# Kernel optimization log

Measured on AMD Instinct MI355X. Metric: run time of the kernel, lower is better.

Reference implementation:

```python
import math
import jax, jax.numpy as jnp
import numpy as np

CAPACITY_FACTOR = 1.0
MIN_CAPACITY = 8


def setup_inputs() -> dict:
    key = jax.random.key(0)
    k1, k2 = jax.random.split(key)
    s, d, e = 8192, 1024, 64
    inputs = jax.random.normal(k1, (s, d), dtype=jnp.float32)
    wg_weight = jax.random.normal(k2, (e, d), dtype=jnp.float32) * (1.0 / math.sqrt(d))
    return {"inputs": inputs, "wg_weight": wg_weight}


def reference(inputs, wg_weight):
    # gate projection (always fp32 in the original)
    logits = inputs.astype(jnp.float32) @ wg_weight.T  # [s, e]
    s, e = logits.shape
    # static capacity: ceil(s/e * capacity_factor), floored at min_capacity
    capacity = max(int(math.ceil(s / e * CAPACITY_FACTOR)), MIN_CAPACITY)

    gates = jax.nn.softmax(logits, axis=1)            # [s, e]
    indices = jnp.argmax(gates, axis=1)               # [s]
    mask = jax.nn.one_hot(indices, e, dtype=jnp.int32)  # [s, e]
    exp_counts = jnp.sum(mask, axis=0)                # [e]

    # load-balancing aux loss (uses mask BEFORE capacity dropping)
    me = jnp.mean(gates, axis=0)
    ce = jnp.mean(mask.astype(jnp.float32), axis=0)
    l_aux = jnp.sum(me * ce) * e

    # capacity dropping: with use_rts=False, topk over the binary mask keeps
    # the first `capacity` tokens routed to each expert, i.e. cumulative
    # position-in-expert < capacity
    positions = jnp.cumsum(mask, axis=0) - 1          # [s, e]
    mask = mask * (positions < capacity).astype(jnp.int32)

    locations = jnp.cumsum(mask, axis=0) - 1          # [s, e]
    locations_s = jnp.sum(locations * mask, axis=1)   # [s] slot per token

    gates = gates * mask.astype(jnp.float32)          # zero out dropped tokens
    locations_sc = jax.nn.one_hot(locations_s, capacity, dtype=jnp.float32)  # [s, c]
    combine_weights = jnp.einsum('se,sc->sec', gates, locations_sc)  # [s, e, c]
    dispatch_mask = combine_weights.astype(bool)
    return l_aux, combine_weights, dispatch_mask, exp_counts
```

## Files before the change

### kernel.cpp

```cpp
#include <hip/hip_runtime.h>
#include <cstdint>
#include <cstddef>

#define S 8192
#define Dm 1024
#define E 64
#define CAP 128
#define SEC 67108864ull

#define GEMM_BLOCKS 256
#define FILL_BLOCKS 1792

typedef float f32x4 __attribute__((ext_vector_type(4)));

__global__ __launch_bounds__(256) void k_main(const float* __restrict__ x,
                                              const float* __restrict__ w,
                                              float* __restrict__ gate,
                                              int* __restrict__ idx,
                                              float* __restrict__ me_part,
                                              float* __restrict__ out) {
    int bid = blockIdx.x;
    int tid = threadIdx.x;
    if (bid < GEMM_BLOCKS) {
        __shared__ float Al[32][66];
        __shared__ float Wl[64][68];
        __shared__ float sm[32];
        __shared__ float sinv[32];
        int tok = tid & 31;
        int eo = tid >> 5;
        int t0 = bid * 32;
        const float* asrc = x + (size_t)(t0 + (tid >> 3)) * Dm + (tid & 7) * 8;
        const float* wsrc0 = w + (size_t)(tid >> 3) * Dm + (tid & 7) * 8;
        const float* wsrc1 = wsrc0 + 32 * (size_t)Dm;
        float* adst = &Al[tid >> 3][(tid & 7) * 8];
        float* wdst0 = &Wl[tid >> 3][(tid & 7) * 8];
        float* wdst1 = &Wl[32 + (tid >> 3)][(tid & 7) * 8];

        float acc[8] = {0.f, 0.f, 0.f, 0.f, 0.f, 0.f, 0.f, 0.f};
        float4 pa0 = *(const float4*)(asrc + 0);
        float4 pa1 = *(const float4*)(asrc + 4);
        float4 pw0 = *(const float4*)(wsrc0 + 0);
        float4 pw1 = *(const float4*)(wsrc0 + 4);
        float4 pw2 = *(const float4*)(wsrc1 + 0);
        float4 pw3 = *(const float4*)(wsrc1 + 4);

        for (int ch = 0; ch < 16; ++ch) {
            __syncthreads();
            *(float2*)(adst + 0) = make_float2(pa0.x, pa0.y);
            *(float2*)(adst + 2) = make_float2(pa0.z, pa0.w);
            *(float2*)(adst + 4) = make_float2(pa1.x, pa1.y);
            *(float2*)(adst + 6) = make_float2(pa1.z, pa1.w);
            *(float4*)(wdst0 + 0) = pw0;
            *(float4*)(wdst0 + 4) = pw1;
            *(float4*)(wdst1 + 0) = pw2;
            *(float4*)(wdst1 + 4) = pw3;
            __syncthreads();
            if (ch < 15) {
                int kb = (ch + 1) * 64;
                pa0 = *(const float4*)(asrc + kb);
                pa1 = *(const float4*)(asrc + kb + 4);
                pw0 = *(const float4*)(wsrc0 + kb);
                pw1 = *(const float4*)(wsrc0 + kb + 4);
                pw2 = *(const float4*)(wsrc1 + kb);
                pw3 = *(const float4*)(wsrc1 + kb + 4);
            }
#pragma unroll 4
            for (int k4 = 0; k4 < 16; ++k4) {
                float2 aa = *(const float2*)&Al[tok][k4 * 4];
                float2 ab = *(const float2*)&Al[tok][k4 * 4 + 2];
#pragma unroll
                for (int j = 0; j < 8; ++j) {
                    float4 wv = *(const float4*)&Wl[eo * 8 + j][k4 * 4];
                    acc[j] = fmaf(ab.y, wv.w, fmaf(ab.x, wv.z,
                             fmaf(aa.y, wv.y, fmaf(aa.x, wv.x, acc[j]))));
                }
            }
        }
        __syncthreads();
#pragma unroll
        for (int j = 0; j < 8; ++j) Al[tok][eo * 8 + j] = acc[j];
        __syncthreads();
        if (tid < 32) {
            float m = Al[tid][0];
            int am = 0;
#pragma unroll
            for (int c = 1; c < E; ++c) {
                float v = Al[tid][c];
                if (v > m) { m = v; am = c; }
            }
            float ssum = 0.f;
#pragma unroll
            for (int c = 0; c < E; ++c) ssum += __expf(Al[tid][c] - m);
            float inv = 1.0f / ssum;
            gate[t0 + tid] = inv;
            idx[t0 + tid] = am;
            sm[tid] = m;
            sinv[tid] = inv;
        }
        __syncthreads();
        if (tid < E) {
            float cs = 0.f;
#pragma unroll 8
            for (int r = 0; r < 32; ++r)
                cs += __expf(Al[r][tid] - sm[r]) * sinv[r];
            me_part[bid * E + tid] = cs;
        }
    } else {
        int fb = bid - GEMM_BLOCKS;
        const unsigned N4 = (unsigned)((1ull + 2ull * SEC + 64ull) / 4ull);
        f32x4 z = {0.f, 0.f, 0.f, 0.f};
        f32x4* o4 = (f32x4*)out;
        for (unsigned i = (unsigned)fb * 256u + tid; i < N4; i += FILL_BLOCKS * 256u)
            o4[i] = z;
    }
}

__global__ __launch_bounds__(256) void k_scan(const int* __restrict__ idx,
                                              const float* __restrict__ gate,
                                              const float* __restrict__ me_part,
                                              float* __restrict__ out) {
    int e = blockIdx.x;
    int tid = threadIdx.x;
    int lane = tid & 63;
    int wid = tid >> 6;
    __shared__ int wsum[4];
    __shared__ float red[256];
    int running = 0;
    for (int ch = 0; ch < S / 256; ++ch) {
        int t = ch * 256 + tid;
        bool f = (idx[t] == e);
        unsigned long long b = __ballot(f);
        int pre = __popcll(b & ((1ull << lane) - 1ull));
        if (lane == 0) wsum[wid] = __popcll(b);
        __syncthreads();
        int off = running;
#pragma unroll
        for (int w2 = 0; w2 < 4; ++w2)
            if (w2 < wid) off += wsum[w2];
        int p = off + pre;
        if (f && p < CAP) {
            size_t o = 1 + (size_t)t * (E * CAP) + (size_t)e * CAP + (size_t)p;
            out[o] = gate[t];
            out[o + (size_t)SEC] = 1.0f;
        }
        running += wsum[0] + wsum[1] + wsum[2] + wsum[3];
        __syncthreads();
    }
    red[tid] = me_part[tid * E + e];
    __syncthreads();
    for (int s2 = 128; s2 > 0; s2 >>= 1) {
        if (tid < s2) red[tid] += red[tid + s2];
        __syncthreads();
    }
    if (tid == 0) {
        out[1 + 2 * (size_t)SEC + e] = (float)running;
        float la = red[0] * (1.0f / (float)S) *
                   ((float)running / (float)S) * (float)E;
        atomicAdd(out, la);
    }
}

extern "C" void kernel_launch(void* const* d_in, const int* in_sizes, int n_in,
                              void* d_out, int out_size, void* d_ws, size_t ws_size,
                              hipStream_t stream) {
    const float* x = (const float*)d_in[0];
    const float* w = (const float*)d_in[1];
    float* out = (float*)d_out;

    float* me_part = (float*)d_ws;
    float* gate = me_part + GEMM_BLOCKS * E;
    int* idx = (int*)(gate + S);

    k_main<<<dim3(GEMM_BLOCKS + FILL_BLOCKS), dim3(256), 0, stream>>>(
        x, w, gate, idx, me_part, out);
    k_scan<<<dim3(64), dim3(256), 0, stream>>>(idx, gate, me_part, out);
}
```

Before: 140.5 us.

## Fuse scan kernel into main kernel using atomic completion counters

Folds the per-expert scan and aux-loss blocks into the main kernel. They spin-wait on a device-scope counter until all gate blocks finish, buffer kept token indices in shared memory, then wait on a second counter for the zero-fill blocks before scattering the writes. This is meant to remove the second kernel launch and its serialization gap, and to overlap the scan with the bulk zero fill. In exchange it adds a memset per call. It also depends on every spin-waiting block and the blocks it waits on being resident at the same time, otherwise it can deadlock.

New measurement: 237.6 us. +69.2%, slower.

```diff
diff --git a/kernel.cpp b/kernel.cpp
--- a/kernel.cpp
+++ b/kernel.cpp
@@ -9,7 +9,8 @@
 #define SEC 67108864ull
 
 #define GEMM_BLOCKS 256
-#define FILL_BLOCKS 1792
+#define SCAN_BLOCKS 64
+#define FILL_BLOCKS 1728
 
 typedef float f32x4 __attribute__((ext_vector_type(4)));
 
@@ -18,6 +19,7 @@
                                               float* __restrict__ gate,
                                               int* __restrict__ idx,
                                               float* __restrict__ me_part,
+                                              unsigned* __restrict__ dcnt,
                                               float* __restrict__ out) {
     int bid = blockIdx.x;
     int tid = threadIdx.x;
@@ -105,58 +107,82 @@
                 cs += __expf(Al[r][tid] - sm[r]) * sinv[r];
             me_part[bid * E + tid] = cs;
         }
+        __syncthreads();
+        if (tid == 0)
+            __hip_atomic_fetch_add(&dcnt[0], 1u, __ATOMIC_RELEASE,
+                                   __HIP_MEMORY_SCOPE_AGENT);
+    } else if (bid < GEMM_BLOCKS + SCAN_BLOCKS) {
+        __shared__ int wsum[4];
+        __shared__ float red[256];
+        __shared__ int kt[CAP];
+        int e = bid - GEMM_BLOCKS;
+        int lane = tid & 63;
+        int wid = tid >> 6;
+        if (tid == 0) {
+            while (__hip_atomic_load(&dcnt[0], __ATOMIC_ACQUIRE,
+                                     __HIP_MEMORY_SCOPE_AGENT) < GEMM_BLOCKS)
+                __builtin_amdgcn_s_sleep(16);
+        }
+        __syncthreads();
+        int running = 0;
+        for (int ch = 0; ch < S / 256; ++ch) {
+            int t = ch * 256 + tid;
+            bool f = (idx[t] == e);
+            unsigned long long b = __ballot(f);
+            int pre = __popcll(b & ((1ull << lane) - 1ull));
+            if (lane == 0) wsum[wid] = __popcll(b);
+            __syncthreads();
+            int off = running;
+#pragma unroll
+            for (int w2 = 0; w2 < 4; ++w2)
+                if (w2 < wid) off += wsum[w2];
+            int p = off + pre;
+            if (f && p < CAP) kt[p] = t;
+            running += wsum[0] + wsum[1] + wsum[2] + wsum[3];
+            __syncthreads();
+        }
+        red[tid] = me_part[tid * E + e];
+        __syncthreads();
+        for (int s2 = 128; s2 > 0; s2 >>= 1) {
+            if (tid < s2) red[tid] += red[tid + s2];
+            __syncthreads();
+        }
+        int nk = running < CAP ? running : CAP;
+        bool wr = tid < nk;
+        size_t o = 0;
+        float gv = 0.f;
+        if (wr) {
+            int t = kt[tid];
+            o = 1 + (size_t)t * (E * CAP) + (size_t)e * CAP + (size_t)tid;
+            gv = gate[t];
+        }
+        if (tid == 0) {
+            while (__hip_atomic_load(&dcnt[1], __ATOMIC_ACQUIRE,
+                                     __HIP_MEMORY_SCOPE_AGENT) < FILL_BLOCKS)
+                __builtin_amdgcn_s_sleep(16);
+        }
+        __syncthreads();
+        if (wr) {
+            out[o] = gv;
+            out[o + SEC] = 1.0f;
+        }
+        if (tid == 0) {
+            out[1 + 2 * SEC + e] = (float)running;
+            float la = red[0] * (1.0f / (float)S) *
+                       ((float)running / (float)S) * (float)E;
+            atomicAdd(out, la);
+        }
     } else {
-        int fb = bid - GEMM_BLOCKS;
+        int fb = bid - (GEMM_BLOCKS + SCAN_BLOCKS);
         const unsigned N4 = (unsigned)((1ull + 2ull * SEC + 64ull) / 4ull);
         f32x4 z = {0.f, 0.f, 0.f, 0.f};
         f32x4* o4 = (f32x4*)out;
         for (unsigned i = (unsigned)fb * 256u + tid; i < N4; i += FILL_BLOCKS * 256u)
             o4[i] = z;
-    }
-}
-
-__global__ __launch_bounds__(256) void k_scan(const int* __restrict__ idx,
-                                              const float* __restrict__ gate,
-                                              const float* __restrict__ me_part,
-                                              float* __restrict__ out) {
-    int e = blockIdx.x;
-    int tid = threadIdx.x;
-    int lane = tid & 63;
-    int wid = tid >> 6;
-    __shared__ int wsum[4];
-    __shared__ float red[256];
-    int running = 0;
-    for (int ch = 0; ch < S / 256; ++ch) {
-        int t = ch * 256 + tid;
-        bool f = (idx[t] == e);
-        unsigned long long b = __ballot(f);
-        int pre = __popcll(b & ((1ull << lane) - 1ull));
-        if (lane == 0) wsum[wid] = __popcll(b);
-        __syncthreads();
-        int off = running;
-#pragma unroll
-        for (int w2 = 0; w2 < 4; ++w2)
-            if (w2 < wid) off += wsum[w2];
-        int p = off + pre;
-        if (f && p < CAP) {
-            size_t o = 1 + (size_t)t * (E * CAP) + (size_t)e * CAP + (size_t)p;
-            out[o] = gate[t];
-            out[o + (size_t)SEC] = 1.0f;
-        }
-        running += wsum[0] + wsum[1] + wsum[2] + wsum[3];
-        __syncthreads();
-    }
-    red[tid] = me_part[tid * E + e];
-    __syncthreads();
-    for (int s2 = 128; s2 > 0; s2 >>= 1) {
-        if (tid < s2) red[tid] += red[tid + s2];
-        __syncthreads();
-    }
-    if (tid == 0) {
-        out[1 + 2 * (size_t)SEC + e] = (float)running;
-        float la = red[0] * (1.0f / (float)S) *
-                   ((float)running / (float)S) * (float)E;
-        atomicAdd(out, la);
+        __syncthreads();
+        if (tid == 0)
+            __hip_atomic_fetch_add(&dcnt[1], 1u, __ATOMIC_RELEASE,
+                                   __HIP_MEMORY_SCOPE_AGENT);
     }
 }
 
@@ -170,8 +196,9 @@
     float* me_part = (float*)d_ws;
     float* gate = me_part + GEMM_BLOCKS * E;
     int* idx = (int*)(gate + S);
-
-    k_main<<<dim3(GEMM_BLOCKS + FILL_BLOCKS), dim3(256), 0, stream>>>(
-        x, w, gate, idx, me_part, out);
-    k_scan<<<dim3(64), dim3(256), 0, stream>>>(idx, gate, me_part, out);
+    unsigned* dcnt = (unsigned*)(idx + S);
+
+    hipMemsetAsync(dcnt, 0, 2 * sizeof(unsigned), stream);
+    k_main<<<dim3(GEMM_BLOCKS + SCAN_BLOCKS + FILL_BLOCKS), dim3(256), 0, stream>>>(
+        x, w, gate, idx, me_part, dcnt, out);
 }
```

## Overlap capacity scan with output zero-fill and defer scatter to separate kernel

Applied to the files above, without the earlier changes.

The GEMM/softmax stage now runs alone. The per-expert capacity scan is launched alongside the large zero-fill of the combine and dispatch tensors. Instead of scattering into the output, the scan writes a per-token (target slot, gate) record, and a small third kernel scatters those records once the fill is done. The aux loss becomes a deterministic shuffle reduction instead of an atomicAdd. The aim is to hide the latency-bound serial scan behind the bandwidth-bound fill, at the cost of an extra launch and of no longer overlapping the fill with the GEMM.

New measurement: 187.9 us. +33.8%, slower.

```diff
diff --git a/kernel.cpp b/kernel.cpp
--- a/kernel.cpp
+++ b/kernel.cpp
@@ -9,154 +9,185 @@
 #define SEC 67108864ull
 
 #define GEMM_BLOCKS 256
-#define FILL_BLOCKS 1792
+#define SCAN_BLOCKS 64
+#define FILL_BLOCKS 1984
+#define N4F 33554432u
 
 typedef float f32x4 __attribute__((ext_vector_type(4)));
 
-__global__ __launch_bounds__(256) void k_main(const float* __restrict__ x,
+__global__ __launch_bounds__(256) void k_gemm(const float* __restrict__ x,
                                               const float* __restrict__ w,
                                               float* __restrict__ gate,
                                               int* __restrict__ idx,
-                                              float* __restrict__ me_part,
-                                              float* __restrict__ out) {
+                                              float* __restrict__ me_part) {
     int bid = blockIdx.x;
     int tid = threadIdx.x;
-    if (bid < GEMM_BLOCKS) {
-        __shared__ float Al[32][66];
-        __shared__ float Wl[64][68];
-        __shared__ float sm[32];
-        __shared__ float sinv[32];
-        int tok = tid & 31;
-        int eo = tid >> 5;
-        int t0 = bid * 32;
-        const float* asrc = x + (size_t)(t0 + (tid >> 3)) * Dm + (tid & 7) * 8;
-        const float* wsrc0 = w + (size_t)(tid >> 3) * Dm + (tid & 7) * 8;
-        const float* wsrc1 = wsrc0 + 32 * (size_t)Dm;
-        float* adst = &Al[tid >> 3][(tid & 7) * 8];
-        float* wdst0 = &Wl[tid >> 3][(tid & 7) * 8];
-        float* wdst1 = &Wl[32 + (tid >> 3)][(tid & 7) * 8];
-
-        float acc[8] = {0.f, 0.f, 0.f, 0.f, 0.f, 0.f, 0.f, 0.f};
-        float4 pa0 = *(const float4*)(asrc + 0);
-        float4 pa1 = *(const float4*)(asrc + 4);
-        float4 pw0 = *(const float4*)(wsrc0 + 0);
-        float4 pw1 = *(const float4*)(wsrc0 + 4);
-        float4 pw2 = *(const float4*)(wsrc1 + 0);
-        float4 pw3 = *(const float4*)(wsrc1 + 4);
-
-        for (int ch = 0; ch < 16; ++ch) {
+    __shared__ float Al[32][66];
+    __shared__ float Wl[64][68];
+    __shared__ float sm[32];
+    __shared__ float sinv[32];
+    int tok = tid & 31;
+    int eo = tid >> 5;
+    int t0 = bid * 32;
+    const float* asrc = x + (size_t)(t0 + (tid >> 3)) * Dm + (tid & 7) * 8;
+    const float* wsrc0 = w + (size_t)(tid >> 3) * Dm + (tid & 7) * 8;
+    const float* wsrc1 = wsrc0 + 32 * (size_t)Dm;
+    float* adst = &Al[tid >> 3][(tid & 7) * 8];
+    float* wdst0 = &Wl[tid >> 3][(tid & 7) * 8];
+    float* wdst1 = &Wl[32 + (tid >> 3)][(tid & 7) * 8];
+
+    float acc[8] = {0.f, 0.f, 0.f, 0.f, 0.f, 0.f, 0.f, 0.f};
+    float4 pa0 = *(const float4*)(asrc + 0);
+    float4 pa1 = *(const float4*)(asrc + 4);
+    float4 pw0 = *(const float4*)(wsrc0 + 0);
+    float4 pw1 = *(const float4*)(wsrc0 + 4);
+    float4 pw2 = *(const float4*)(wsrc1 + 0);
+    float4 pw3 = *(const float4*)(wsrc1 + 4);
+
+    for (int ch = 0; ch < 16; ++ch) {
+        __syncthreads();
+        *(float2*)(adst + 0) = make_float2(pa0.x, pa0.y);
+        *(float2*)(adst + 2) = make_float2(pa0.z, pa0.w);
+        *(float2*)(adst + 4) = make_float2(pa1.x, pa1.y);
+        *(float2*)(adst + 6) = make_float2(pa1.z, pa1.w);
+        *(float4*)(wdst0 + 0) = pw0;
+        *(float4*)(wdst0 + 4) = pw1;
+        *(float4*)(wdst1 + 0) = pw2;
+        *(float4*)(wdst1 + 4) = pw3;
+        __syncthreads();
+        if (ch < 15) {
+            int kb = (ch + 1) * 64;
+            pa0 = *(const float4*)(asrc + kb);
+            pa1 = *(const float4*)(asrc + kb + 4);
+            pw0 = *(const float4*)(wsrc0 + kb);
+            pw1 = *(const float4*)(wsrc0 + kb + 4);
+            pw2 = *(const float4*)(wsrc1 + kb);
+            pw3 = *(const float4*)(wsrc1 + kb + 4);
+        }
+#pragma unroll 4
+        for (int k4 = 0; k4 < 16; ++k4) {
+            float2 aa = *(const float2*)&Al[tok][k4 * 4];
+            float2 ab = *(const float2*)&Al[tok][k4 * 4 + 2];
+#pragma unroll
+            for (int j = 0; j < 8; ++j) {
+                float4 wv = *(const float4*)&Wl[eo * 8 + j][k4 * 4];
+                acc[j] = fmaf(ab.y, wv.w, fmaf(ab.x, wv.z,
+                         fmaf(aa.y, wv.y, fmaf(aa.x, wv.x, acc[j]))));
+            }
+        }
+    }
+    __syncthreads();
+#pragma unroll
+    for (int j = 0; j < 8; ++j) Al[tok][eo * 8 + j] = acc[j];
+    __syncthreads();
+    if (tid < 32) {
+        float m = Al[tid][0];
+        int am = 0;
+#pragma unroll
+        for (int c = 1; c < E; ++c) {
+            float v = Al[tid][c];
+            if (v > m) { m = v; am = c; }
+        }
+        float ssum = 0.f;
+#pragma unroll
+        for (int c = 0; c < E; ++c) ssum += __expf(Al[tid][c] - m);
+        float inv = 1.0f / ssum;
+        gate[t0 + tid] = inv;
+        idx[t0 + tid] = am;
+        sm[tid] = m;
+        sinv[tid] = inv;
+    }
+    __syncthreads();
+    if (tid < E) {
+        float cs = 0.f;
+#pragma unroll 8
+        for (int r = 0; r < 32; ++r)
+            cs += __expf(Al[r][tid] - sm[r]) * sinv[r];
+        me_part[bid * E + tid] = cs;
+    }
+}
+
+__global__ __launch_bounds__(256) void k_fillscan(const int* __restrict__ idx,
+                                                  const float* __restrict__ gate,
+                                                  const float* __restrict__ me_part,
+                                                  float2* __restrict__ tg,
+                                                  float* __restrict__ la_part,
+                                                  float* __restrict__ out) {
+    int bid = blockIdx.x;
+    int tid = threadIdx.x;
+    if (bid < SCAN_BLOCKS) {
+        __shared__ int wsum[4];
+        __shared__ float red[256];
+        int e = bid;
+        int lane = tid & 63;
+        int wid = tid >> 6;
+        if (bid == 0 && tid == 0) {
+            out[1] = 0.f; out[2] = 0.f; out[3] = 0.f;
+            out[2 * SEC] = 0.f;
+        }
+        int running = 0;
+        for (int ch = 0; ch < S / 256; ++ch) {
+            int t = ch * 256 + tid;
+            bool f = (idx[t] == e);
+            unsigned long long b = __ballot(f);
+            int pre = __popcll(b & ((1ull << lane) - 1ull));
+            if (lane == 0) wsum[wid] = __popcll(b);
             __syncthreads();
-            *(float2*)(adst + 0) = make_float2(pa0.x, pa0.y);
-            *(float2*)(adst + 2) = make_float2(pa0.z, pa0.w);
-            *(float2*)(adst + 4) = make_float2(pa1.x, pa1.y);
-            *(float2*)(adst + 6) = make_float2(pa1.z, pa1.w);
-            *(float4*)(wdst0 + 0) = pw0;
-            *(float4*)(wdst0 + 4) = pw1;
-            *(float4*)(wdst1 + 0) = pw2;
-            *(float4*)(wdst1 + 4) = pw3;
+            int off = running;
+#pragma unroll
+            for (int w2 = 0; w2 < 4; ++w2)
+                if (w2 < wid) off += wsum[w2];
+            int p = off + pre;
+            if (f) {
+                int tgt = (p < CAP) ? e * CAP + p : -1;
+                tg[t] = make_float2(__int_as_float(tgt), gate[t]);
+            }
+            running += wsum[0] + wsum[1] + wsum[2] + wsum[3];
             __syncthreads();
-            if (ch < 15) {
-                int kb = (ch + 1) * 64;
-                pa0 = *(const float4*)(asrc + kb);
-                pa1 = *(const float4*)(asrc + kb + 4);
-                pw0 = *(const float4*)(wsrc0 + kb);
-                pw1 = *(const float4*)(wsrc0 + kb + 4);
-                pw2 = *(const float4*)(wsrc1 + kb);
-                pw3 = *(const float4*)(wsrc1 + kb + 4);
-            }
-#pragma unroll 4
-            for (int k4 = 0; k4 < 16; ++k4) {
-                float2 aa = *(const float2*)&Al[tok][k4 * 4];
-                float2 ab = *(const float2*)&Al[tok][k4 * 4 + 2];
-#pragma unroll
-                for (int j = 0; j < 8; ++j) {
-                    float4 wv = *(const float4*)&Wl[eo * 8 + j][k4 * 4];
-                    acc[j] = fmaf(ab.y, wv.w, fmaf(ab.x, wv.z,
-                             fmaf(aa.y, wv.y, fmaf(aa.x, wv.x, acc[j]))));
-                }
-            }
-        }
+        }
+        red[tid] = me_part[tid * E + e];
         __syncthreads();
-#pragma unroll
-        for (int j = 0; j < 8; ++j) Al[tok][eo * 8 + j] = acc[j];
-        __syncthreads();
-        if (tid < 32) {
-            float m = Al[tid][0];
-            int am = 0;
-#pragma unroll
-            for (int c = 1; c < E; ++c) {
-                float v = Al[tid][c];
-                if (v > m) { m = v; am = c; }
-            }
-            float ssum = 0.f;
-#pragma unroll
-            for (int c = 0; c < E; ++c) ssum += __expf(Al[tid][c] - m);
-            float inv = 1.0f / ssum;
-            gate[t0 + tid] = inv;
-            idx[t0 + tid] = am;
-            sm[tid] = m;
-            sinv[tid] = inv;
-        }
-        __syncthreads();
-        if (tid < E) {
-            float cs = 0.f;
-#pragma unroll 8
-            for (int r = 0; r < 32; ++r)
-                cs += __expf(Al[r][tid] - sm[r]) * sinv[r];
-            me_part[bid * E + tid] = cs;
+        for (int s2 = 128; s2 > 0; s2 >>= 1) {
+            if (tid < s2) red[tid] += red[tid + s2];
+            __syncthreads();
+        }
+        if (tid == 0) {
+            out[1 + 2 * SEC + e] = (float)running;
+            la_part[e] = red[0] * (1.0f / (float)S) *
+                         ((float)running / (float)S) * (float)E;
         }
     } else {
-        int fb = bid - GEMM_BLOCKS;
-        const unsigned N4 = (unsigned)((1ull + 2ull * SEC + 64ull) / 4ull);
+        int fb = bid - SCAN_BLOCKS;
         f32x4 z = {0.f, 0.f, 0.f, 0.f};
         f32x4* o4 = (f32x4*)out;
-        for (unsigned i = (unsigned)fb * 256u + tid; i < N4; i += FILL_BLOCKS * 256u)
+        for (unsigned i = 1u + (unsigned)fb * 256u + tid; i < N4F;
+             i += FILL_BLOCKS * 256u)
             o4[i] = z;
     }
 }
 
-__global__ __launch_bounds__(256) void k_scan(const int* __restrict__ idx,
-                                              const float* __restrict__ gate,
-                                              const float* __restrict__ me_part,
-                                              float* __restrict__ out) {
-    int e = blockIdx.x;
+__global__ __launch_bounds__(256) void k_scatter(const float2* __restrict__ tg,
+                                                 const float* __restrict__ la_part,
+                                                 float* __restrict__ out) {
+    int bid = blockIdx.x;
     int tid = threadIdx.x;
-    int lane = tid & 63;
-    int wid = tid >> 6;
-    __shared__ int wsum[4];
-    __shared__ float red[256];
-    int running = 0;
-    for (int ch = 0; ch < S / 256; ++ch) {
-        int t = ch * 256 + tid;
-        bool f = (idx[t] == e);
-        unsigned long long b = __ballot(f);
-        int pre = __popcll(b & ((1ull << lane) - 1ull));
-        if (lane == 0) wsum[wid] = __popcll(b);
-        __syncthreads();
-        int off = running;
-#pragma unroll
-        for (int w2 = 0; w2 < 4; ++w2)
-            if (w2 < wid) off += wsum[w2];
-        int p = off + pre;
-        if (f && p < CAP) {
-            size_t o = 1 + (size_t)t * (E * CAP) + (size_t)e * CAP + (size_t)p;
-            out[o] = gate[t];
-            out[o + (size_t)SEC] = 1.0f;
-        }
-        running += wsum[0] + wsum[1] + wsum[2] + wsum[3];
-        __syncthreads();
-    }
-    red[tid] = me_part[tid * E + e];
-    __syncthreads();
-    for (int s2 = 128; s2 > 0; s2 >>= 1) {
-        if (tid < s2) red[tid] += red[tid + s2];
-        __syncthreads();
-    }
-    if (tid == 0) {
-        out[1 + 2 * (size_t)SEC + e] = (float)running;
-        float la = red[0] * (1.0f / (float)S) *
-                   ((float)running / (float)S) * (float)E;
-        atomicAdd(out, la);
+    if (bid == 32) {
+        if (tid < E) {
+            float la = la_part[tid];
+#pragma unroll
+            for (int off = 32; off > 0; off >>= 1)
+                la += __shfl_down(la, off, 64);
+            if (tid == 0) out[0] = la;
+        }
+        return;
+    }
+    int t = bid * 256 + tid;
+    float2 g = tg[t];
+    int tgt = __float_as_int(g.x);
+    if (tgt >= 0) {
+        size_t o = 1 + (size_t)t * (E * CAP) + (size_t)tgt;
+        out[o] = g.y;
+        out[o + SEC] = 1.0f;
     }
 }
 
@@ -170,8 +201,11 @@
     float* me_part = (float*)d_ws;
     float* gate = me_part + GEMM_BLOCKS * E;
     int* idx = (int*)(gate + S);
-
-    k_main<<<dim3(GEMM_BLOCKS + FILL_BLOCKS), dim3(256), 0, stream>>>(
-        x, w, gate, idx, me_part, out);
-    k_scan<<<dim3(64), dim3(256), 0, stream>>>(idx, gate, me_part, out);
-}
+    float2* tg = (float2*)(idx + S);
+    float* la_part = (float*)(tg + S);
+
+    k_gemm<<<dim3(GEMM_BLOCKS), dim3(256), 0, stream>>>(x, w, gate, idx, me_part);
+    k_fillscan<<<dim3(SCAN_BLOCKS + FILL_BLOCKS), dim3(256), 0, stream>>>(
+        idx, gate, me_part, tg, la_part, out);
+    k_scatter<<<dim3(33), dim3(256), 0, stream>>>(tg, la_part, out);
+}
```

## Split GEMM K-loop across two thread groups and retune zero-fill grid

Applied to the files above, without the earlier changes.

Doubles the block size to 512 threads. In the GEMM blocks, each 256-thread half now handles one half of the K dimension with its own shared-memory tiles, and the halves combine partial sums through shared memory before the softmax. This halves the serial K-loop per block so the gate projection finishes sooner. The zero-fill branch now uses 512 blocks of 512 threads instead of 1792 of 256, giving fewer fill threads in flight and doubling shared memory per GEMM block.

After: 146.7 us. 4.4% more time.

```diff
diff --git a/kernel.cpp b/kernel.cpp
--- a/kernel.cpp
+++ b/kernel.cpp
@@ -9,11 +9,13 @@
 #define SEC 67108864ull
 
 #define GEMM_BLOCKS 256
-#define FILL_BLOCKS 1792
+#define FILL_BLOCKS 512
+#define NTHR 512
+#define N4ALL 33554448u
 
 typedef float f32x4 __attribute__((ext_vector_type(4)));
 
-__global__ __launch_bounds__(256) void k_main(const float* __restrict__ x,
+__global__ __launch_bounds__(512) void k_main(const float* __restrict__ x,
                                               const float* __restrict__ w,
                                               float* __restrict__ gate,
                                               int* __restrict__ idx,
@@ -22,19 +24,22 @@
     int bid = blockIdx.x;
     int tid = threadIdx.x;
     if (bid < GEMM_BLOCKS) {
-        __shared__ float Al[32][66];
-        __shared__ float Wl[64][68];
+        __shared__ float Al[2][32][66];
+        __shared__ float Wl[2][64][68];
         __shared__ float sm[32];
         __shared__ float sinv[32];
-        int tok = tid & 31;
-        int eo = tid >> 5;
+        int g = tid >> 8;
+        int lt = tid & 255;
+        int tok = lt & 31;
+        int eo = lt >> 5;
         int t0 = bid * 32;
-        const float* asrc = x + (size_t)(t0 + (tid >> 3)) * Dm + (tid & 7) * 8;
-        const float* wsrc0 = w + (size_t)(tid >> 3) * Dm + (tid & 7) * 8;
+        int kb0 = g * 512;
+        const float* asrc = x + (size_t)(t0 + (lt >> 3)) * Dm + kb0 + (lt & 7) * 8;
+        const float* wsrc0 = w + (size_t)(lt >> 3) * Dm + kb0 + (lt & 7) * 8;
         const float* wsrc1 = wsrc0 + 32 * (size_t)Dm;
-        float* adst = &Al[tid >> 3][(tid & 7) * 8];
-        float* wdst0 = &Wl[tid >> 3][(tid & 7) * 8];
-        float* wdst1 = &Wl[32 + (tid >> 3)][(tid & 7) * 8];
+        float* adst = &Al[g][lt >> 3][(lt & 7) * 8];
+        float* wdst0 = &Wl[g][lt >> 3][(lt & 7) * 8];
+        float* wdst1 = &Wl[g][32 + (lt >> 3)][(lt & 7) * 8];
 
         float acc[8] = {0.f, 0.f, 0.f, 0.f, 0.f, 0.f, 0.f, 0.f};
         float4 pa0 = *(const float4*)(asrc + 0);
@@ -44,7 +49,7 @@
         float4 pw2 = *(const float4*)(wsrc1 + 0);
         float4 pw3 = *(const float4*)(wsrc1 + 4);
 
-        for (int ch = 0; ch < 16; ++ch) {
+        for (int ch = 0; ch < 8; ++ch) {
             __syncthreads();
             *(float2*)(adst + 0) = make_float2(pa0.x, pa0.y);
             *(float2*)(adst + 2) = make_float2(pa0.z, pa0.w);
@@ -55,7 +60,7 @@
             *(float4*)(wdst1 + 0) = pw2;
             *(float4*)(wdst1 + 4) = pw3;
             __syncthreads();
-            if (ch < 15) {
+            if (ch < 7) {
                 int kb = (ch + 1) * 64;
                 pa0 = *(const float4*)(asrc + kb);
                 pa1 = *(const float4*)(asrc + kb + 4);
@@ -66,31 +71,39 @@
             }
 #pragma unroll 4
             for (int k4 = 0; k4 < 16; ++k4) {
-                float2 aa = *(const float2*)&Al[tok][k4 * 4];
-                float2 ab = *(const float2*)&Al[tok][k4 * 4 + 2];
+                float2 aa = *(const float2*)&Al[g][tok][k4 * 4];
+                float2 ab = *(const float2*)&Al[g][tok][k4 * 4 + 2];
 #pragma unroll
                 for (int j = 0; j < 8; ++j) {
-                    float4 wv = *(const float4*)&Wl[eo * 8 + j][k4 * 4];
+                    float4 wv = *(const float4*)&Wl[g][eo * 8 + j][k4 * 4];
                     acc[j] = fmaf(ab.y, wv.w, fmaf(ab.x, wv.z,
                              fmaf(aa.y, wv.y, fmaf(aa.x, wv.x, acc[j]))));
                 }
             }
         }
         __syncthreads();
+        if (g == 1) {
 #pragma unroll
-        for (int j = 0; j < 8; ++j) Al[tok][eo * 8 + j] = acc[j];
+            for (int j = 0; j < 8; ++j) Al[1][tok][eo * 8 + j] = acc[j];
+        }
+        __syncthreads();
+        if (g == 0) {
+#pragma unroll
+            for (int j = 0; j < 8; ++j)
+                Al[0][tok][eo * 8 + j] = acc[j] + Al[1][tok][eo * 8 + j];
+        }
         __syncthreads();
         if (tid < 32) {
-            float m = Al[tid][0];
+            float m = Al[0][tid][0];
             int am = 0;
 #pragma unroll
             for (int c = 1; c < E; ++c) {
-                float v = Al[tid][c];
+                float v = Al[0][tid][c];
                 if (v > m) { m = v; am = c; }
             }
             float ssum = 0.f;
 #pragma unroll
-            for (int c = 0; c < E; ++c) ssum += __expf(Al[tid][c] - m);
+            for (int c = 0; c < E; ++c) ssum += __expf(Al[0][tid][c] - m);
             float inv = 1.0f / ssum;
             gate[t0 + tid] = inv;
             idx[t0 + tid] = am;
@@ -102,15 +115,15 @@
             float cs = 0.f;
 #pragma unroll 8
             for (int r = 0; r < 32; ++r)
-                cs += __expf(Al[r][tid] - sm[r]) * sinv[r];
+                cs += __expf(Al[0][r][tid] - sm[r]) * sinv[r];
             me_part[bid * E + tid] = cs;
         }
     } else {
         int fb = bid - GEMM_BLOCKS;
-        const unsigned N4 = (unsigned)((1ull + 2ull * SEC + 64ull) / 4ull);
         f32x4 z = {0.f, 0.f, 0.f, 0.f};
         f32x4* o4 = (f32x4*)out;
-        for (unsigned i = (unsigned)fb * 256u + tid; i < N4; i += FILL_BLOCKS * 256u)
+        for (unsigned i = (unsigned)fb * NTHR + tid; i < N4ALL;
+             i += FILL_BLOCKS * NTHR)
             o4[i] = z;
     }
 }
@@ -170,8 +183,10 @@
     float* me_part = (float*)d_ws;
     float* gate = me_part + GEMM_BLOCKS * E;
     int* idx = (int*)(gate + S);
+    float* me_sum = (float*)(idx + S);
+    (void)me_sum;
 
-    k_main<<<dim3(GEMM_BLOCKS + FILL_BLOCKS), dim3(256), 0, stream>>>(
+    k_main<<<dim3(GEMM_BLOCKS + FILL_BLOCKS), dim3(NTHR), 0, stream>>>(
         x, w, gate, idx, me_part, out);
     k_scan<<<dim3(64), dim3(256), 0, stream>>>(idx, gate, me_part, out);
 }
```
